# Performance work log

Measured on AMD Instinct MI355X. Metric: run time of the kernel, lower is better.

Reference implementation:

```python
import math
import jax
import jax.numpy as jnp
import numpy as np

B, N, NPOINT, K = 8, 2048, 512, 16
CIN = 64
MLP = [64, 128, 256]
M_W = 8    # PAConv weight-bank size
HID = 16   # scorenet hidden width
GEOM = 10  # 3 rel-xyz + 1 dist + 3 norm + 3 angles


def setup_inputs():
    key = jax.random.key(0)
    ks = jax.random.split(key, 40)
    inp = {}
    inp['xyz'] = jax.random.normal(ks[0], (B, 3, N), jnp.float32)
    inp['norm'] = jax.random.normal(ks[1], (B, 3, N), jnp.float32)
    inp['X_axis'] = jax.random.normal(ks[2], (B, 3, N), jnp.float32)
    inp['Y_axis'] = jax.random.normal(ks[3], (B, 3, N), jnp.float32)
    inp['points'] = jax.random.normal(ks[4], (B, CIN, N), jnp.float32) * 0.5
    cin = CIN
    ki = 5
    for l, cout in enumerate(MLP):
        inp['w1_%d' % l] = jax.random.normal(ks[ki], (HID, GEOM), jnp.float32) / np.sqrt(GEOM); ki += 1
        inp['b1_%d' % l] = jnp.zeros((HID,), jnp.float32)
        inp['w2_%d' % l] = jax.random.normal(ks[ki], (M_W, HID), jnp.float32) / np.sqrt(HID); ki += 1
        inp['b2_%d' % l] = jnp.zeros((M_W,), jnp.float32)
        inp['bank_%d' % l] = jax.random.normal(ks[ki], (M_W, cin, cout), jnp.float32) / np.sqrt(cin); ki += 1
        if l < len(MLP) - 1:
            inp['gamma_%d' % l] = jnp.ones((cout,), jnp.float32)
            inp['beta_%d' % l] = jnp.zeros((cout,), jnp.float32)
        cin = cout
    return inp


def _group(t, idx):
    # t: (B, C, N), idx: (B, ...) int -> (B, C, ...)
    return jax.vmap(lambda p, i: p[:, i])(t, idx)


def _fps(xyz_t, npoint):
    # xyz_t: (B, N, 3) -> (B, npoint) int32; standard iterative FPS starting at index 0
    b, n, _ = xyz_t.shape
    def body(i, c):
        idxs, dists, far = c
        idxs = idxs.at[:, i].set(far)
        centroid = jnp.take_along_axis(xyz_t, far[:, None, None], axis=1)  # (B,1,3)
        d = jnp.sum((xyz_t - centroid) ** 2, axis=-1)
        dists = jnp.minimum(dists, d)
        return idxs, dists, jnp.argmax(dists, axis=-1).astype(jnp.int32)
    idxs = jnp.zeros((b, npoint), jnp.int32)
    dists = jnp.full((b, n), 1e10, xyz_t.dtype)
    far = jnp.zeros((b,), jnp.int32)
    idxs, _, _ = jax.lax.fori_loop(0, npoint, body, (idxs, dists, far))
    return idxs


def _sqdist(a, b):
    # a: (B, P, 3), b: (B, N, 3) -> (B, P, N)
    return (jnp.sum(a ** 2, -1)[:, :, None] + jnp.sum(b ** 2, -1)[:, None, :]
            - 2.0 * jnp.einsum('bpc,bnc->bpn', a, b))


def _angles(gxyz, gn, gX, gY):
    # all (B, 3, P, K) -> (B, 3, P, K); normalized angles to z(norm)/x/y frame axes
    nn = jnp.linalg.norm(gxyz, axis=1)
    def ang(v):
        c = jnp.sum(gxyz * v, axis=1) / (nn * jnp.linalg.norm(v, axis=1) + 1e-8)
        return jnp.arccos(jnp.clip(c, -1.0, 1.0)) / math.pi
    return jnp.stack([ang(gn), ang(gX), ang(gY)], axis=1)


def _paconv(geom, feats, w1, b1, w2, b2, bank, gamma=None, beta=None, act=True):
    # ScoreNet over geometric channels -> softmax scores over M weight matrices
    h = jax.nn.relu(jnp.einsum('hg,bgpk->bhpk', w1, geom) + b1[None, :, None, None])
    s = jax.nn.softmax(jnp.einsum('mh,bhpk->bmpk', w2, h) + b2[None, :, None, None], axis=1)
    out = jnp.einsum('bcpk,mco,bmpk->bopk', feats, bank, s)
    if gamma is not None:
        mu = out.mean(axis=(0, 2, 3), keepdims=True)
        var = out.var(axis=(0, 2, 3), keepdims=True)
        out = (out - mu) / jnp.sqrt(var + 1e-5) * gamma[None, :, None, None] + beta[None, :, None, None]
    return jax.nn.relu(out) if act else out


def reference(xyz, norm, X_axis, Y_axis, points,
              w1_0, b1_0, w2_0, b2_0, bank_0, gamma_0, beta_0,
              w1_1, b1_1, w2_1, b2_1, bank_1, gamma_1, beta_1,
              w1_2, b1_2, w2_2, b2_2, bank_2):
    xyz_t = jnp.transpose(xyz, (0, 2, 1))           # (B,N,3)
    fidx = _fps(xyz_t, NPOINT)                      # (B,NPOINT)
    new_xyz = _group(xyz, fidx)                     # (B,3,NPOINT)
    sq = _sqdist(jnp.transpose(new_xyz, (0, 2, 1)), xyz_t)  # (B,NPOINT,N)
    idx = jax.lax.top_k(-sq, K)[1]                  # (B,NPOINT,K) ascending distance
    grouped_xyz = _group(xyz, idx) - new_xyz[:, :, :, None]  # (B,3,NPOINT,K)
    dist = jnp.sqrt(jnp.sum(grouped_xyz ** 2, axis=1) + 1e-10)  # (B,NPOINT,K)
    dmin = dist.min(axis=2, keepdims=True)
    dist = (dist - dmin) / (dist.max(axis=2, keepdims=True) - dmin + 1e-10)
    new_points = _group(points, idx)                # (B,CIN,NPOINT,K)
    grouped_norm = _group(norm, idx)
    grouped_X = _group(X_axis, idx)
    grouped_Y = _group(Y_axis, idx)
    grouped_angles = _angles(grouped_xyz, grouped_norm, grouped_X, grouped_Y)
    new_norm = grouped_norm[:, :, :, 0]
    new_X = grouped_X[:, :, :, 0]
    new_Y = grouped_Y[:, :, :, 0]
    geom = jnp.concatenate([grouped_xyz, dist[:, None], grouped_norm, grouped_angles], axis=1)  # (B,10,NPOINT,K)
    new_points = _paconv(geom, new_points, w1_0, b1_0, w2_0, b2_0, bank_0, gamma_0, beta_0, act=True)
    new_points = _paconv(geom, new_points, w1_1, b1_1, w2_1, b2_1, bank_1, gamma_1, beta_1, act=True)
    new_points = _paconv(geom, new_points, w1_2, b1_2, w2_2, b2_2, bank_2, None, None, act=False)
    new_points = jnp.max(new_points, axis=3)        # (B,MLP[-1],NPOINT)
    return (new_xyz, new_norm, new_X, new_Y, new_points)
```

## Files before the change

### kernel.cpp

```cpp
#include <hip/hip_runtime.h>
#include <math.h>

#define NBATCH 8
#define NPTS   2048
#define NPOINT 512
#define KNB    16
#define NROWS  (NBATCH*NPOINT*KNB)

typedef unsigned short ushort_t;
typedef unsigned int   uint_t;
typedef unsigned long long ull_t;
typedef __attribute__((ext_vector_type(8))) short  short8;
typedef __attribute__((ext_vector_type(4))) float  f32x4;
typedef __attribute__((ext_vector_type(2))) float  f32x2;

#define B0_OFF 0
#define B1_OFF 32768
#define B2_OFF 98304
#define BT_TOT 360448

#define LDS_BARRIER() asm volatile("s_waitcnt lgkmcnt(0)\n\ts_barrier" ::: "memory")

__device__ __align__(16) int      g_fidx[NBATCH * NPOINT];
__device__ __align__(16) int      g_knn [NROWS];
__device__ __align__(16) float    g_sums[1024];
__device__ __align__(16) float    g_pT  [NBATCH * NPTS * 64];
__device__ __align__(16) float    g_S   [(size_t)3 * NROWS * 8];
__device__ __align__(16) float    g_act1[(size_t)NROWS * 64];
__device__ __align__(16) float    g_act2[(size_t)NROWS * 128];
__device__ __align__(16) ushort_t g_bankF[BT_TOT];

__device__ __forceinline__ ushort_t f2bf(float f) {
    uint_t u = __float_as_uint(f);
    return (ushort_t)((u + 0x7FFFu + ((u >> 16) & 1u)) >> 16);
}

template<int CTRL>
__device__ __forceinline__ ull_t dpp_u64(ull_t k) {
    int lo = (int)(uint_t)k;
    int hi = (int)(uint_t)(k >> 32);
    int slo = __builtin_amdgcn_update_dpp(0, lo, CTRL, 0xF, 0xF, true);
    int shi = __builtin_amdgcn_update_dpp(0, hi, CTRL, 0xF, 0xF, true);
    return ((ull_t)(uint_t)shi << 32) | (uint_t)slo;
}

__device__ __forceinline__ ull_t dpp_max_u64(ull_t key) {
    { ull_t s = dpp_u64<0x111>(key); if (s > key) key = s; }
    { ull_t s = dpp_u64<0x112>(key); if (s > key) key = s; }
    { ull_t s = dpp_u64<0x114>(key); if (s > key) key = s; }
    { ull_t s = dpp_u64<0x118>(key); if (s > key) key = s; }
    { ull_t s = dpp_u64<0x142>(key); if (s > key) key = s; }
    { ull_t s = dpp_u64<0x143>(key); if (s > key) key = s; }
    return key;
}

template<int CTRL>
__device__ __forceinline__ uint_t dpp_u32(uint_t v) {
    return (uint_t)__builtin_amdgcn_update_dpp(0, (int)v, CTRL, 0xF, 0xF, true);
}

__device__ __forceinline__ uint_t dpp_max_u32(uint_t v) {
    { uint_t s = dpp_u32<0x111>(v); if (s > v) v = s; }
    { uint_t s = dpp_u32<0x112>(v); if (s > v) v = s; }
    { uint_t s = dpp_u32<0x114>(v); if (s > v) v = s; }
    { uint_t s = dpp_u32<0x118>(v); if (s > v) v = s; }
    { uint_t s = dpp_u32<0x142>(v); if (s > v) v = s; }
    { uint_t s = dpp_u32<0x143>(v); if (s > v) v = s; }
    return v;
}

template<int COUT>
__device__ __forceinline__ void bank_frag(const float* __restrict__ bank,
                                          ushort_t* __restrict__ dst, int e) {
    const int j = e & 7;
    const int lane = (e >> 3) & 63;
    const int rem = e >> 9;
    constexpr int NTL = COUT / 16;
    const int nt = rem % NTL;
    const int kc = rem / NTL;
    const int q = lane >> 4, nlo = lane & 15;
    const int k = kc * 32 + q * 8 + j;
    const int n = nt * 16 + nlo;
    dst[e] = f2bf(bank[(size_t)k * COUT + n]);
}

__global__ __launch_bounds__(256) void front_kernel(const float* __restrict__ xyz,
                                                    const float* __restrict__ points,
                                                    const float* __restrict__ bank0,
                                                    const float* __restrict__ bank1,
                                                    const float* __restrict__ bank2) {
    __shared__ float smem[4 * NPTS];
    __shared__ ull_t s_key[2][4];
    const int bid = blockIdx.x;
    const int t = threadIdx.x;

    if (bid >= NBATCH) {
        if (bid < NBATCH + 256) {
            float (*tile)[65] = reinterpret_cast<float(*)[65]>(smem);
            const int blk = bid - NBATCH;
            const int b = blk >> 5;
            const int n0 = (blk & 31) * 64;
            const int lane = t & 63, q = t >> 6;
            #pragma unroll
            for (int i = 0; i < 16; ++i) {
                int c = q * 16 + i;
                tile[c][lane] = points[(b * 64 + c) * NPTS + n0 + lane];
            }
            __syncthreads();
            #pragma unroll
            for (int i = 0; i < 16; ++i) {
                int n = q * 16 + i;
                g_pT[(size_t)(b * NPTS + n0 + n) * 64 + lane] = tile[lane][n];
            }
        } else if (bid == NBATCH + 256) {
            g_sums[t] = 0.0f;
            g_sums[256 + t] = 0.0f;
            g_sums[512 + t] = 0.0f;
            g_sums[768 + t] = 0.0f;
        } else {
            const int e = (bid - (NBATCH + 257)) * 256 + t;
            if (e < 32768) {
                bank_frag<64>(bank0, g_bankF + B0_OFF, e);
            } else if (e < 98304) {
                bank_frag<128>(bank1, g_bankF + B1_OFF, e - 32768);
            } else {
                bank_frag<256>(bank2, g_bankF + B2_OFF, e - 98304);
            }
        }
        return;
    }

    {
        #pragma clang fp contract(off)
        const int b = bid;
        const int lane = t & 63, w = t >> 6;
        const float* xb = xyz + b * 3 * NPTS;
        float4* s_pt = reinterpret_cast<float4*>(smem);
        f32x2 xp[4], yp[4], zp[4];
        float d[8];
        {
            const float4* xq = reinterpret_cast<const float4*>(xb + t * 8);
            const float4* yq = reinterpret_cast<const float4*>(xb + NPTS + t * 8);
            const float4* zq = reinterpret_cast<const float4*>(xb + 2 * NPTS + t * 8);
            float4 a0 = xq[0], a1 = xq[1];
            float4 b0 = yq[0], b1 = yq[1];
            float4 c0 = zq[0], c1 = zq[1];
            xp[0] = (f32x2){a0.x, a0.y}; xp[1] = (f32x2){a0.z, a0.w};
            xp[2] = (f32x2){a1.x, a1.y}; xp[3] = (f32x2){a1.z, a1.w};
            yp[0] = (f32x2){b0.x, b0.y}; yp[1] = (f32x2){b0.z, b0.w};
            yp[2] = (f32x2){b1.x, b1.y}; yp[3] = (f32x2){b1.z, b1.w};
            zp[0] = (f32x2){c0.x, c0.y}; zp[1] = (f32x2){c0.z, c0.w};
            zp[2] = (f32x2){c1.x, c1.y}; zp[3] = (f32x2){c1.z, c1.w};
            float4 p0; float4 p1; float4 p2; float4 p3;
            float4 p4; float4 p5; float4 p6; float4 p7;
            p0.x = a0.x; p0.y = b0.x; p0.z = c0.x; p0.w = 0.f;
            p1.x = a0.y; p1.y = b0.y; p1.z = c0.y; p1.w = 0.f;
            p2.x = a0.z; p2.y = b0.z; p2.z = c0.z; p2.w = 0.f;
            p3.x = a0.w; p3.y = b0.w; p3.z = c0.w; p3.w = 0.f;
            p4.x = a1.x; p4.y = b1.x; p4.z = c1.x; p4.w = 0.f;
            p5.x = a1.y; p5.y = b1.y; p5.z = c1.y; p5.w = 0.f;
            p6.x = a1.z; p6.y = b1.z; p6.z = c1.z; p6.w = 0.f;
            p7.x = a1.w; p7.y = b1.w; p7.z = c1.w; p7.w = 0.f;
            s_pt[t * 8 + 0] = p0; s_pt[t * 8 + 1] = p1;
            s_pt[t * 8 + 2] = p2; s_pt[t * 8 + 3] = p3;
            s_pt[t * 8 + 4] = p4; s_pt[t * 8 + 5] = p5;
            s_pt[t * 8 + 6] = p6; s_pt[t * 8 + 7] = p7;
            #pragma unroll
            for (int j = 0; j < 8; ++j) d[j] = 1e10f;
        }
        __syncthreads();
        int far = 0;
        for (int i = 0; i < NPOINT; ++i) {
            if (t == 0) g_fidx[b * NPOINT + i] = far;
            const float4 c4 = s_pt[far];
            const f32x2 cxp = (f32x2){c4.x, c4.x};
            const f32x2 cyp = (f32x2){c4.y, c4.y};
            const f32x2 czp = (f32x2){c4.z, c4.z};
            uint_t bb = 0u;
            #pragma unroll
            for (int a = 0; a < 4; ++a) {
                f32x2 dx = xp[a] - cxp;
                f32x2 dy = yp[a] - cyp;
                f32x2 dz = zp[a] - czp;
                f32x2 s2 = dx*dx + dy*dy;
                s2 = s2 + dz*dz;
                float dn0 = fminf(d[2*a],   s2[0]);
                float dn1 = fminf(d[2*a+1], s2[1]);
                d[2*a] = dn0; d[2*a+1] = dn1;
                uint_t u0 = __float_as_uint(dn0);
                uint_t u1 = __float_as_uint(dn1);
                bb = (u0 > bb) ? u0 : bb;
                bb = (u1 > bb) ? u1 : bb;
            }
            uint_t wm = dpp_max_u32(bb);
            const uint_t wbits = (uint_t)__builtin_amdgcn_readlane((int)wm, 63);
            int li = 8;
            #pragma unroll
            for (int j = 7; j >= 0; --j)
                li = (__float_as_uint(d[j]) == wbits) ? j : li;
            ull_t mk = __ballot(li < 8);
            const int fl = __ffsll((unsigned long long)mk) - 1;
            const int wj = __builtin_amdgcn_readlane(li, fl);
            const int wp = (((w << 6) + fl) << 3) + wj;
            if (lane == 0) s_key[i & 1][w] = ((ull_t)wbits << 32) | (uint_t)(~wp);
            LDS_BARRIER();
            const ull_t* kb = s_key[i & 1];
            ull_t k0 = kb[0], k1 = kb[1], k2 = kb[2], k3 = kb[3];
            if (k1 > k0) k0 = k1;
            if (k3 > k2) k2 = k3;
            if (k2 > k0) k0 = k2;
            far = (int)(~(uint_t)k0) & (NPTS - 1);
        }
    }
}

__global__ __launch_bounds__(256) void knn_score_kernel(
    const float* __restrict__ xyz, const float* __restrict__ nrm,
    const float* __restrict__ Xa, const float* __restrict__ Ya,
    const float* __restrict__ w1_0, const float* __restrict__ b1_0,
    const float* __restrict__ w2_0, const float* __restrict__ b2_0,
    const float* __restrict__ w1_1, const float* __restrict__ b1_1,
    const float* __restrict__ w2_1, const float* __restrict__ b2_1,
    const float* __restrict__ w1_2, const float* __restrict__ b1_2,
    const float* __restrict__ w2_2, const float* __restrict__ b2_2) {
    __shared__ float w1s[3][16][10];
    __shared__ float b1s[3][16];
    __shared__ float w2s[3][8][16];
    __shared__ float b2s[3][8];
    const int t = threadIdx.x;
    {
        const float* w1p[3] = {w1_0, w1_1, w1_2};
        const float* b1p[3] = {b1_0, b1_1, b1_2};
        const float* w2p[3] = {w2_0, w2_1, w2_2};
        const float* b2p[3] = {b2_0, b2_1, b2_2};
        #pragma unroll
        for (int l = 0; l < 3; ++l) {
            if (t < 160) w1s[l][t / 10][t % 10] = w1p[l][t];
            if (t < 16)  b1s[l][t] = b1p[l][t];
            if (t < 128) w2s[l][t / 16][t % 16] = w2p[l][t];
            if (t < 8)   b2s[l][t] = b2p[l][t];
        }
    }
    __syncthreads();

    const int wave = blockIdx.x * 4 + (t >> 6);
    const int lane = t & 63;
    const int b = wave >> 9;
    const float* xb = xyz + b * 3 * NPTS;
    const int fi = g_fidx[wave] & (NPTS - 1);
    int nmine = 0;

    {
        #pragma clang fp contract(off)
        float ax = xb[fi];
        float ay = xb[NPTS + fi];
        float az = xb[2*NPTS + fi];
        float sa = ax*ax + ay*ay; sa = sa + az*az;
        float d[32];
        #pragma unroll
        for (int j = 0; j < 32; ++j) {
            int pp = j * 64 + lane;
            float bx = xb[pp];
            float by = xb[NPTS + pp];
            float bz = xb[2*NPTS + pp];
            float sb = bx*bx + by*by; sb = sb + bz*bz;
            float dot = ax*bx + ay*by; dot = dot + az*bz;
            float t1 = sa + sb;
            float t2 = 2.0f * dot;
            d[j] = t1 - t2;
        }
        for (int r = 0; r < KNB; ++r) {
            float best = 1e30f; int bi = 0x7fffffff;
            #pragma unroll
            for (int j = 0; j < 32; ++j) {
                if (d[j] < best) { best = d[j]; bi = j * 64 + lane; }
            }
            uint_t ub = __float_as_uint(best);
            ub = (ub & 0x80000000u) ? ~ub : (ub | 0x80000000u);
            ull_t key = ((ull_t)(~ub) << 32) | (uint_t)(~bi);
            key = dpp_max_u64(key);
            uint_t wlo = (uint_t)__builtin_amdgcn_readlane((int)(uint_t)key, 63);
            bi = (int)(~wlo) & (NPTS - 1);
            if (lane == 0) g_knn[wave * KNB + r] = bi;
            if (lane == r) nmine = bi;
            int rl = bi & 63, rs = bi >> 6;
            if (lane == rl) {
                #pragma unroll
                for (int j = 0; j < 32; ++j) if (j == rs) d[j] = 1e30f;
            }
        }
    }

    if (lane < 16) {
        const int row = wave * KNB + lane;
        const int n = nmine & (NPTS - 1);
        const float* nb = nrm + b * 3 * NPTS;
        const float* Xb = Xa  + b * 3 * NPTS;
        const float* Yb = Ya  + b * 3 * NPTS;
        float gx, gy, gz, sq, draw, nnv;
        {
            #pragma clang fp contract(off)
            gx = xb[n]        - xb[fi];
            gy = xb[NPTS + n] - xb[NPTS + fi];
            gz = xb[2*NPTS+n] - xb[2*NPTS+fi];
            sq = gx*gx + gy*gy;
            sq = sq + gz*gz;
            draw = sqrtf(sq + 1e-10f);
            nnv = sqrtf(sq);
        }
        float dmin = draw, dmax = draw;
        #pragma unroll
        for (int m = 1; m < 16; m <<= 1) {
            dmin = fminf(dmin, __shfl_xor(dmin, m, 16));
            dmax = fmaxf(dmax, __shfl_xor(dmax, m, 16));
        }
        float dist;
        {
            #pragma clang fp contract(off)
            dist = (draw - dmin) / ((dmax - dmin) + 1e-10f);
        }
        float nx = nb[n], ny = nb[NPTS+n], nz = nb[2*NPTS+n];
        float Xx = Xb[n], Xy = Xb[NPTS+n], Xz = Xb[2*NPTS+n];
        float Yx = Yb[n], Yy = Yb[NPTS+n], Yz = Yb[2*NPTS+n];
        float g[10];
        g[0]=gx; g[1]=gy; g[2]=gz; g[3]=dist; g[4]=nx; g[5]=ny; g[6]=nz;
        {
            float vs[3][3] = {{nx,ny,nz},{Xx,Xy,Xz},{Yx,Yy,Yz}};
            #pragma unroll
            for (int a = 0; a < 3; ++a) {
                float vx=vs[a][0], vy=vs[a][1], vz=vs[a][2];
                float dot, nv;
                {
                    #pragma clang fp contract(off)
                    dot = gx*vx + gy*vy; dot = dot + gz*vz;
                    float s2 = vx*vx + vy*vy; s2 = s2 + vz*vz;
                    nv = sqrtf(s2);
                }
                float cc = dot / (nnv * nv + 1e-8f);
                cc = fminf(1.0f, fmaxf(-1.0f, cc));
                g[7+a] = acosf(cc) / 3.14159274101257324f;
            }
        }
        #pragma unroll
        for (int l = 0; l < 3; ++l) {
            float h[16];
            #pragma unroll
            for (int i = 0; i < 16; ++i) {
                float a = b1s[l][i];
                #pragma unroll
                for (int j = 0; j < 10; ++j) a += w1s[l][i][j] * g[j];
                h[i] = fmaxf(a, 0.0f);
            }
            float e[8]; float mx = -1e30f;
            #pragma unroll
            for (int m = 0; m < 8; ++m) {
                float a = b2s[l][m];
                #pragma unroll
                for (int j = 0; j < 16; ++j) a += w2s[l][m][j] * h[j];
                e[m] = a; mx = fmaxf(mx, a);
            }
            float sum = 0.0f;
            #pragma unroll
            for (int m = 0; m < 8; ++m) { e[m] = expf(e[m] - mx); sum += e[m]; }
            #pragma unroll
            for (int m = 0; m < 8; ++m)
                g_S[(size_t)l * NROWS * 8 + (size_t)row * 8 + m] = e[m] / sum;
        }
    }
}

template<int LAYER, int CIN, int COUT>
__global__ __launch_bounds__(256) void gemm_kernel(const float* __restrict__ gamma,
                                                   const float* __restrict__ beta,
                                                   float* __restrict__ dout,
                                                   const float* __restrict__ xyz,
                                                   const float* __restrict__ nrm,
                                                   const float* __restrict__ Xa,
                                                   const float* __restrict__ Ya) {
    if constexpr (LAYER == 0) {
        if (blockIdx.x >= 1024) {
            const int g = (blockIdx.x - 1024) * 256 + threadIdx.x;
            const int b = g / NPOINT, p = g % NPOINT;
            const int fi = g_fidx[g] & (NPTS - 1);
            const int n0 = g_knn[g * KNB] & (NPTS - 1);
            #pragma unroll
            for (int a = 0; a < 3; ++a) {
                dout[            (b*3 + a) * NPOINT + p] = xyz[(b*3 + a) * NPTS + fi];
                dout[12288 +     (b*3 + a) * NPOINT + p] = nrm[(b*3 + a) * NPTS + n0];
                dout[24576 +     (b*3 + a) * NPOINT + p] = Xa [(b*3 + a) * NPTS + n0];
                dout[36864 +     (b*3 + a) * NPOINT + p] = Ya [(b*3 + a) * NPTS + n0];
            }
            return;
        }
    }

    const float* __restrict__ A = (LAYER == 0) ? g_pT : (LAYER == 1) ? g_act1 : g_act2;
    float* __restrict__ O = (LAYER == 0) ? g_act1 : (LAYER == 1) ? g_act2 : dout;
    constexpr int NTT = COUT / 16;
    constexpr int NTW = NTT / 4;
    constexpr int CCM = CIN / 32;
    constexpr int BOFF = (LAYER == 0) ? B0_OFF : (LAYER == 1) ? B1_OFF : B2_OFF;
    __shared__ ushort_t As[2][64][36];
    __shared__ float s_scale[(LAYER >= 1) ? CIN : 1];
    __shared__ float s_shift[(LAYER >= 1) ? CIN : 1];
    __shared__ float s_rs[(LAYER < 2) ? COUT : 1];
    __shared__ float s_rss[(LAYER < 2) ? COUT : 1];

    const int t = threadIdx.x;
    const int lane = t & 63, w = t >> 6;
    const int q = lane >> 4, nlo = lane & 15;
    const int row0 = blockIdx.x * 64;
    const int arow_i = t >> 2, acg = t & 3;

    if constexpr (LAYER >= 1) {
        const float* sb = (LAYER == 1) ? g_sums : (g_sums + 256);
        if (t < CIN) {
            float mu  = sb[t] * (1.0f / 65536.0f);
            float var = sb[CIN + t] * (1.0f / 65536.0f) - mu * mu;
            var = fmaxf(var, 0.0f);
            float sc = gamma[t] / sqrtf(var + 1e-5f);
            s_scale[t] = sc;
            s_shift[t] = beta[t] - mu * sc;
        }
        __syncthreads();
    }

    size_t arow;
    if (LAYER == 0) {
        const int row = row0 + arow_i;
        const int b = row >> 13;
        const int n = g_knn[row] & (NPTS - 1);
        arow = (size_t)(b * NPTS + n) * 64;
    } else {
        arow = (size_t)(row0 + arow_i) * CIN;
    }
    const float* Sbase = g_S + (size_t)LAYER * NROWS * 8 + (size_t)(row0 + arow_i) * 8;

    float svv[8];
    #pragma unroll
    for (int m = 0; m < 8; ++m) svv[m] = Sbase[m];

    f32x4 acc[4][NTW];
    #pragma unroll
    for (int mi = 0; mi < 4; ++mi)
        #pragma unroll
        for (int ni = 0; ni < NTW; ++ni) acc[mi][ni] = (f32x4){0.f, 0.f, 0.f, 0.f};

    const ushort_t* fbase = g_bankF + BOFF + lane * 8;

    union FragU { uint4 u4; uint2 u2[2]; short8 s; };
    FragU B[2][NTW];
    #pragma unroll
    for (int ni = 0; ni < NTW; ++ni)
        B[0][ni].u4 = *reinterpret_cast<const uint4*>(fbase + (size_t)(w * NTW + ni) * 512);

    float vraw[8], vnext[8];
    {
        const float* ap = A + arow + acg * 8;
        float4 fa = *reinterpret_cast<const float4*>(ap);
        float4 fb = *reinterpret_cast<const float4*>(ap + 4);
        vraw[0]=fa.x; vraw[1]=fa.y; vraw[2]=fa.z; vraw[3]=fa.w;
        vraw[4]=fb.x; vraw[5]=fb.y; vraw[6]=fb.z; vraw[7]=fb.w;
    }

    int par = 0;
    for (int cc = 0; cc < CCM; ++cc) {
        float v[8];
        #pragma unroll
        for (int j = 0; j < 8; ++j) {
            if constexpr (LAYER >= 1) {
                const int c = cc * 32 + acg * 8 + j;
                v[j] = fmaxf(vraw[j] * s_scale[c] + s_shift[c], 0.f);
            } else {
                v[j] = vraw[j];
            }
        }
        #pragma unroll
        for (int m = 0; m < 8; ++m) {
            {
                const float sv = svv[m];
                uint_t* dst = reinterpret_cast<uint_t*>(&As[par][arow_i][acg * 8]);
                #pragma unroll
                for (int j = 0; j < 8; j += 2)
                    dst[j >> 1] = (uint_t)f2bf(sv * v[j]) | ((uint_t)f2bf(sv * v[j+1]) << 16);
            }
            if (m == 0) {
                const int ccn = (cc + 1 < CCM) ? cc + 1 : cc;
                const float* ap = A + arow + ccn * 32 + acg * 8;
                float4 fa = *reinterpret_cast<const float4*>(ap);
                float4 fb = *reinterpret_cast<const float4*>(ap + 4);
                vnext[0]=fa.x; vnext[1]=fa.y; vnext[2]=fa.z; vnext[3]=fa.w;
                vnext[4]=fb.x; vnext[5]=fb.y; vnext[6]=fb.z; vnext[7]=fb.w;
            }
            {
                const int kcn = (m < 7) ? ((m + 1) * CCM + cc)
                                        : ((cc + 1 < CCM) ? (cc + 1) : 0);
                #pragma unroll
                for (int ni = 0; ni < NTW; ++ni)
                    B[(m + 1) & 1][ni].u4 = *reinterpret_cast<const uint4*>(
                        fbase + (size_t)(kcn * NTT + w * NTW + ni) * 512);
            }
            LDS_BARRIER();
            FragU af[4];
            #pragma unroll
            for (int mi = 0; mi < 4; ++mi) {
                af[mi].u2[0] = *reinterpret_cast<const uint2*>(&As[par][mi*16 + nlo][q*8]);
                af[mi].u2[1] = *reinterpret_cast<const uint2*>(&As[par][mi*16 + nlo][q*8 + 4]);
            }
            #pragma unroll
            for (int ni = 0; ni < NTW; ++ni)
                #pragma unroll
                for (int mi = 0; mi < 4; ++mi)
                    acc[mi][ni] = __builtin_amdgcn_mfma_f32_16x16x32_bf16(
                        af[mi].s, B[m & 1][ni].s, acc[mi][ni], 0, 0, 0);
            par ^= 1;
        }
        #pragma unroll
        for (int j = 0; j < 8; ++j) vraw[j] = vnext[j];
    }

    if constexpr (LAYER == 2) {
        const int bp0 = row0 >> 4;
        #pragma unroll
        for (int mi = 0; mi < 4; ++mi) {
            const int bp = bp0 + mi;
            const int b = bp >> 9, p = bp & 511;
            #pragma unroll
            for (int ni = 0; ni < NTW; ++ni) {
                float mv = fmaxf(fmaxf(acc[mi][ni][0], acc[mi][ni][1]),
                                 fmaxf(acc[mi][ni][2], acc[mi][ni][3]));
                mv = fmaxf(mv, __shfl_xor(mv, 16));
                mv = fmaxf(mv, __shfl_xor(mv, 32));
                if (lane < 16) {
                    const int col = w * 64 + ni * 16 + nlo;
                    O[(size_t)(b * 256 + col) * NPOINT + p] = mv;
                }
            }
        }
    } else {
        #pragma unroll
        for (int mi = 0; mi < 4; ++mi)
            #pragma unroll
            for (int ni = 0; ni < NTW; ++ni)
                #pragma unroll
                for (int r2 = 0; r2 < 4; ++r2)
                    O[(size_t)(row0 + mi*16 + q*4 + r2) * COUT + w*NTW*16 + ni*16 + nlo] = acc[mi][ni][r2];
        #pragma unroll
        for (int ni = 0; ni < NTW; ++ni) {
            float s = 0.f, ss = 0.f;
            #pragma unroll
            for (int mi = 0; mi < 4; ++mi) {
                #pragma unroll
                for (int r2 = 0; r2 < 4; ++r2) {
                    float x = acc[mi][ni][r2];
                    s += x; ss += x * x;
                }
            }
            s  += __shfl_xor(s, 16);  s  += __shfl_xor(s, 32);
            ss += __shfl_xor(ss, 16); ss += __shfl_xor(ss, 32);
            if (q == 0) {
                const int c = w * NTW * 16 + ni * 16 + nlo;
                s_rs[c] = s;
                s_rss[c] = ss;
            }
        }
        __syncthreads();
        if (t < COUT) {
            float* sb = (LAYER == 0) ? g_sums : (g_sums + 256);
            atomicAdd(&sb[t], s_rs[t]);
            atomicAdd(&sb[COUT + t], s_rss[t]);
        }
    }
}

extern "C" void kernel_launch(void* const* d_in, const int* in_sizes, int n_in,
                              void* d_out, int out_size, void* d_ws, size_t ws_size,
                              hipStream_t stream) {
    const float* xyz    = (const float*)d_in[0];
    const float* nrm    = (const float*)d_in[1];
    const float* Xa     = (const float*)d_in[2];
    const float* Ya     = (const float*)d_in[3];
    const float* points = (const float*)d_in[4];
    const float* w1_0 = (const float*)d_in[5];  const float* b1_0 = (const float*)d_in[6];
    const float* w2_0 = (const float*)d_in[7];  const float* b2_0 = (const float*)d_in[8];
    const float* bank0 = (const float*)d_in[9];
    const float* g0 = (const float*)d_in[10];   const float* be0 = (const float*)d_in[11];
    const float* w1_1 = (const float*)d_in[12]; const float* b1_1 = (const float*)d_in[13];
    const float* w2_1 = (const float*)d_in[14]; const float* b2_1 = (const float*)d_in[15];
    const float* bank1 = (const float*)d_in[16];
    const float* g1 = (const float*)d_in[17];   const float* be1 = (const float*)d_in[18];
    const float* w1_2 = (const float*)d_in[19]; const float* b1_2 = (const float*)d_in[20];
    const float* w2_2 = (const float*)d_in[21]; const float* b2_2 = (const float*)d_in[22];
    const float* bank2 = (const float*)d_in[23];
    float* out = (float*)d_out;
    (void)d_ws; (void)ws_size; (void)in_sizes; (void)n_in; (void)out_size;

    front_kernel<<<1673, 256, 0, stream>>>(xyz, points, bank0, bank1, bank2);
    knn_score_kernel<<<1024, 256, 0, stream>>>(xyz, nrm, Xa, Ya,
                                               w1_0, b1_0, w2_0, b2_0,
                                               w1_1, b1_1, w2_1, b2_1,
                                               w1_2, b1_2, w2_2, b2_2);
    gemm_kernel<0, 64, 64><<<1040, 256, 0, stream>>>(nullptr, nullptr, out, xyz, nrm, Xa, Ya);
    gemm_kernel<1, 64, 128><<<1024, 256, 0, stream>>>(g0, be0, nullptr, nullptr, nullptr, nullptr, nullptr);
    gemm_kernel<2, 128, 256><<<1024, 256, 0, stream>>>(g1, be1, out + 49152, nullptr, nullptr, nullptr, nullptr);
}
```

Baseline: 461.6 us.

## Fuse FPS and KNN/scorenet into one kernel with per-centroid ready flags

Merges the front kernel (FPS, transpose, bank conversion) and the KNN/scorenet kernel into one launch. KNN waves spin on per-centroid ready flags that the FPS blocks publish each iteration, so neighbour search and scoring overlap the serial FPS loop instead of waiting for it to finish. The FPS shared-memory layout also changes from padded float4 to SoA. The risks are deadlock if KNN blocks occupy every slot before the FPS blocks are scheduled, the cost of spin-polling, and the relaxed atomics giving no ordering guarantee on g_fidx.

```diff
diff --git a/kernel.cpp b/kernel.cpp
--- a/kernel.cpp
+++ b/kernel.cpp
@@ -6,6 +6,12 @@
 #define NPOINT 512
 #define KNB    16
 #define NROWS  (NBATCH*NPOINT*KNB)
+
+#define TRANS_BASE  NBATCH
+#define ZERO_BID    (NBATCH + 256)
+#define CONV_BASE   (NBATCH + 257)
+#define KNN_BASE    (NBATCH + 257 + 1408)
+#define MEGA_GRID   (KNN_BASE + 1024)
 
 typedef unsigned short ushort_t;
 typedef unsigned int   uint_t;
@@ -21,7 +27,8 @@
 
 #define LDS_BARRIER() asm volatile("s_waitcnt lgkmcnt(0)\n\ts_barrier" ::: "memory")
 
-__device__ __align__(16) int      g_fidx[NBATCH * NPOINT];
+__device__ __align__(16) int      g_fidx [NBATCH * NPOINT];
+__device__ __align__(16) int      g_fready[NBATCH * NPOINT];
 __device__ __align__(16) int      g_knn [NROWS];
 __device__ __align__(16) float    g_sums[1024];
 __device__ __align__(16) float    g_pT  [NBATCH * NPTS * 64];
@@ -84,20 +91,27 @@
     dst[e] = f2bf(bank[(size_t)k * COUT + n]);
 }
 
-__global__ __launch_bounds__(256) void front_kernel(const float* __restrict__ xyz,
-                                                    const float* __restrict__ points,
-                                                    const float* __restrict__ bank0,
-                                                    const float* __restrict__ bank1,
-                                                    const float* __restrict__ bank2) {
-    __shared__ float smem[4 * NPTS];
+__global__ __launch_bounds__(256, 5) void mega_kernel(
+    const float* __restrict__ xyz, const float* __restrict__ points,
+    const float* __restrict__ bank0, const float* __restrict__ bank1,
+    const float* __restrict__ bank2,
+    const float* __restrict__ nrm, const float* __restrict__ Xa,
+    const float* __restrict__ Ya,
+    const float* __restrict__ w1_0, const float* __restrict__ b1_0,
+    const float* __restrict__ w2_0, const float* __restrict__ b2_0,
+    const float* __restrict__ w1_1, const float* __restrict__ b1_1,
+    const float* __restrict__ w2_1, const float* __restrict__ b2_1,
+    const float* __restrict__ w1_2, const float* __restrict__ b1_2,
+    const float* __restrict__ w2_2, const float* __restrict__ b2_2) {
+    __shared__ float smem[3 * NPTS];
     __shared__ ull_t s_key[2][4];
     const int bid = blockIdx.x;
     const int t = threadIdx.x;
 
     if (bid >= NBATCH) {
-        if (bid < NBATCH + 256) {
+        if (bid < ZERO_BID) {
             float (*tile)[65] = reinterpret_cast<float(*)[65]>(smem);
-            const int blk = bid - NBATCH;
+            const int blk = bid - TRANS_BASE;
             const int b = blk >> 5;
             const int n0 = (blk & 31) * 64;
             const int lane = t & 63, q = t >> 6;
@@ -112,13 +126,15 @@
                 int n = q * 16 + i;
                 g_pT[(size_t)(b * NPTS + n0 + n) * 64 + lane] = tile[lane][n];
             }
-        } else if (bid == NBATCH + 256) {
+            return;
+        } else if (bid == ZERO_BID) {
             g_sums[t] = 0.0f;
             g_sums[256 + t] = 0.0f;
             g_sums[512 + t] = 0.0f;
             g_sums[768 + t] = 0.0f;
-        } else {
-            const int e = (bid - (NBATCH + 257)) * 256 + t;
+            return;
+        } else if (bid < KNN_BASE) {
+            const int e = (bid - CONV_BASE) * 256 + t;
             if (e < 32768) {
                 bank_frag<64>(bank0, g_bankF + B0_OFF, e);
             } else if (e < 98304) {
@@ -126,6 +142,158 @@
             } else {
                 bank_frag<256>(bank2, g_bankF + B2_OFF, e - 98304);
             }
+            return;
+        }
+
+        {
+            const float* w1p[3] = {w1_0, w1_1, w1_2};
+            const float* b1p[3] = {b1_0, b1_1, b1_2};
+            const float* w2p[3] = {w2_0, w2_1, w2_2};
+            const float* b2p[3] = {b2_0, b2_1, b2_2};
+            #pragma unroll
+            for (int l = 0; l < 3; ++l) {
+                if (t < 160) smem[l * 160 + t] = w1p[l][t];
+                if (t < 16)  smem[480 + l * 16 + t] = b1p[l][t];
+                if (t < 128) smem[528 + l * 128 + t] = w2p[l][t];
+                if (t < 8)   smem[912 + l * 8 + t] = b2p[l][t];
+            }
+        }
+        __syncthreads();
+
+        const int wave = (bid - KNN_BASE) * 4 + (t >> 6);
+        const int lane = t & 63;
+        const int b = wave >> 9;
+        const float* xb = xyz + b * 3 * NPTS;
+
+        int fv = __hip_atomic_load(&g_fready[wave], __ATOMIC_RELAXED,
+                                   __HIP_MEMORY_SCOPE_AGENT);
+        while (fv == 0) {
+            __builtin_amdgcn_s_sleep(8);
+            fv = __hip_atomic_load(&g_fready[wave], __ATOMIC_RELAXED,
+                                   __HIP_MEMORY_SCOPE_AGENT);
+        }
+        if (lane == 0)
+            __hip_atomic_store(&g_fready[wave], 0, __ATOMIC_RELAXED,
+                               __HIP_MEMORY_SCOPE_AGENT);
+        const int fi = (fv - 1) & (NPTS - 1);
+        int nmine = 0;
+
+        {
+            #pragma clang fp contract(off)
+            float ax = xb[fi];
+            float ay = xb[NPTS + fi];
+            float az = xb[2*NPTS + fi];
+            float sa = ax*ax + ay*ay; sa = sa + az*az;
+            float d[32];
+            #pragma unroll
+            for (int j = 0; j < 32; ++j) {
+                int pp = j * 64 + lane;
+                float bx = xb[pp];
+                float by = xb[NPTS + pp];
+                float bz = xb[2*NPTS + pp];
+                float sb = bx*bx + by*by; sb = sb + bz*bz;
+                float dot = ax*bx + ay*by; dot = dot + az*bz;
+                float t1 = sa + sb;
+                float t2 = 2.0f * dot;
+                d[j] = t1 - t2;
+            }
+            for (int r = 0; r < KNB; ++r) {
+                float best = 1e30f; int bi = 0x7fffffff;
+                #pragma unroll
+                for (int j = 0; j < 32; ++j) {
+                    if (d[j] < best) { best = d[j]; bi = j * 64 + lane; }
+                }
+                uint_t ub = __float_as_uint(best);
+                ub = (ub & 0x80000000u) ? ~ub : (ub | 0x80000000u);
+                ull_t key = ((ull_t)(~ub) << 32) | (uint_t)(~bi);
+                key = dpp_max_u64(key);
+                uint_t wlo = (uint_t)__builtin_amdgcn_readlane((int)(uint_t)key, 63);
+                bi = (int)(~wlo) & (NPTS - 1);
+                if (lane == 0) g_knn[wave * KNB + r] = bi;
+                if (lane == r) nmine = bi;
+                int rl = bi & 63, rs = bi >> 6;
+                if (lane == rl) {
+                    #pragma unroll
+                    for (int j = 0; j < 32; ++j) if (j == rs) d[j] = 1e30f;
+                }
+            }
+        }
+
+        if (lane < 16) {
+            const int row = wave * KNB + lane;
+            const int n = nmine & (NPTS - 1);
+            const float* nb = nrm + b * 3 * NPTS;
+            const float* Xb = Xa  + b * 3 * NPTS;
+            const float* Yb = Ya  + b * 3 * NPTS;
+            float gx, gy, gz, sq, draw, nnv;
+            {
+                #pragma clang fp contract(off)
+                gx = xb[n]        - xb[fi];
+                gy = xb[NPTS + n] - xb[NPTS + fi];
+                gz = xb[2*NPTS+n] - xb[2*NPTS+fi];
+                sq = gx*gx + gy*gy;
+                sq = sq + gz*gz;
+                draw = sqrtf(sq + 1e-10f);
+                nnv = sqrtf(sq);
+            }
+            float dmin = draw, dmax = draw;
+            #pragma unroll
+            for (int m = 1; m < 16; m <<= 1) {
+                dmin = fminf(dmin, __shfl_xor(dmin, m, 16));
+                dmax = fmaxf(dmax, __shfl_xor(dmax, m, 16));
+            }
+            float dist;
+            {
+                #pragma clang fp contract(off)
+                dist = (draw - dmin) / ((dmax - dmin) + 1e-10f);
+            }
+            float nx = nb[n], ny = nb[NPTS+n], nz = nb[2*NPTS+n];
+            float Xx = Xb[n], Xy = Xb[NPTS+n], Xz = Xb[2*NPTS+n];
+            float Yx = Yb[n], Yy = Yb[NPTS+n], Yz = Yb[2*NPTS+n];
+            float g[10];
+            g[0]=gx; g[1]=gy; g[2]=gz; g[3]=dist; g[4]=nx; g[5]=ny; g[6]=nz;
+            {
+                float vs[3][3] = {{nx,ny,nz},{Xx,Xy,Xz},{Yx,Yy,Yz}};
+                #pragma unroll
+                for (int a = 0; a < 3; ++a) {
+                    float vx=vs[a][0], vy=vs[a][1], vz=vs[a][2];
+                    float dot, nv;
+                    {
+                        #pragma clang fp contract(off)
+                        dot = gx*vx + gy*vy; dot = dot + gz*vz;
+                        float s2 = vx*vx + vy*vy; s2 = s2 + vz*vz;
+                        nv = sqrtf(s2);
+                    }
+                    float cc = dot / (nnv * nv + 1e-8f);
+                    cc = fminf(1.0f, fmaxf(-1.0f, cc));
+                    g[7+a] = acosf(cc) / 3.14159274101257324f;
+                }
+            }
+            #pragma unroll
+            for (int l = 0; l < 3; ++l) {
+                float h[16];
+                #pragma unroll
+                for (int i = 0; i < 16; ++i) {
+                    float a = smem[480 + l * 16 + i];
+                    #pragma unroll
+                    for (int j = 0; j < 10; ++j) a += smem[l * 160 + i * 10 + j] * g[j];
+                    h[i] = fmaxf(a, 0.0f);
+                }
+                float e[8]; float mx = -1e30f;
+                #pragma unroll
+                for (int m = 0; m < 8; ++m) {
+                    float a = smem[912 + l * 8 + m];
+                    #pragma unroll
+                    for (int j = 0; j < 16; ++j) a += smem[528 + l * 128 + m * 16 + j] * h[j];
+                    e[m] = a; mx = fmaxf(mx, a);
+                }
+                float sum = 0.0f;
+                #pragma unroll
+                for (int m = 0; m < 8; ++m) { e[m] = expf(e[m] - mx); sum += e[m]; }
+                #pragma unroll
+                for (int m = 0; m < 8; ++m)
+                    g_S[(size_t)l * NROWS * 8 + (size_t)row * 8 + m] = e[m] / sum;
+            }
         }
         return;
     }
@@ -135,7 +303,9 @@
         const int b = bid;
         const int lane = t & 63, w = t >> 6;
         const float* xb = xyz + b * 3 * NPTS;
-        float4* s_pt = reinterpret_cast<float4*>(smem);
+        float* s_x = smem;
+        float* s_y = smem + NPTS;
+        float* s_z = smem + 2 * NPTS;
         f32x2 xp[4], yp[4], zp[4];
         float d[8];
         {
@@ -151,31 +321,27 @@
             yp[2] = (f32x2){b1.x, b1.y}; yp[3] = (f32x2){b1.z, b1.w};
             zp[0] = (f32x2){c0.x, c0.y}; zp[1] = (f32x2){c0.z, c0.w};
             zp[2] = (f32x2){c1.x, c1.y}; zp[3] = (f32x2){c1.z, c1.w};
-            float4 p0; float4 p1; float4 p2; float4 p3;
-            float4 p4; float4 p5; float4 p6; float4 p7;
-            p0.x = a0.x; p0.y = b0.x; p0.z = c0.x; p0.w = 0.f;
-            p1.x = a0.y; p1.y = b0.y; p1.z = c0.y; p1.w = 0.f;
-            p2.x = a0.z; p2.y = b0.z; p2.z = c0.z; p2.w = 0.f;
-            p3.x = a0.w; p3.y = b0.w; p3.z = c0.w; p3.w = 0.f;
-            p4.x = a1.x; p4.y = b1.x; p4.z = c1.x; p4.w = 0.f;
-            p5.x = a1.y; p5.y = b1.y; p5.z = c1.y; p5.w = 0.f;
-            p6.x = a1.z; p6.y = b1.z; p6.z = c1.z; p6.w = 0.f;
-            p7.x = a1.w; p7.y = b1.w; p7.z = c1.w; p7.w = 0.f;
-            s_pt[t * 8 + 0] = p0; s_pt[t * 8 + 1] = p1;
-            s_pt[t * 8 + 2] = p2; s_pt[t * 8 + 3] = p3;
-            s_pt[t * 8 + 4] = p4; s_pt[t * 8 + 5] = p5;
-            s_pt[t * 8 + 6] = p6; s_pt[t * 8 + 7] = p7;
+            *reinterpret_cast<float4*>(s_x + t * 8)     = a0;
+            *reinterpret_cast<float4*>(s_x + t * 8 + 4) = a1;
+            *reinterpret_cast<float4*>(s_y + t * 8)     = b0;
+            *reinterpret_cast<float4*>(s_y + t * 8 + 4) = b1;
+            *reinterpret_cast<float4*>(s_z + t * 8)     = c0;
+            *reinterpret_cast<float4*>(s_z + t * 8 + 4) = c1;
             #pragma unroll
             for (int j = 0; j < 8; ++j) d[j] = 1e10f;
         }
         __syncthreads();
         int far = 0;
         for (int i = 0; i < NPOINT; ++i) {
-            if (t == 0) g_fidx[b * NPOINT + i] = far;
-            const float4 c4 = s_pt[far];
-            const f32x2 cxp = (f32x2){c4.x, c4.x};
-            const f32x2 cyp = (f32x2){c4.y, c4.y};
-            const f32x2 czp = (f32x2){c4.z, c4.z};
+            if (t == 0) {
+                g_fidx[b * NPOINT + i] = far;
+                __hip_atomic_store(&g_fready[b * NPOINT + i], far + 1,
+                                   __ATOMIC_RELAXED, __HIP_MEMORY_SCOPE_AGENT);
+            }
+            const float cx = s_x[far], cy = s_y[far], cz = s_z[far];
+            const f32x2 cxp = (f32x2){cx, cx};
+            const f32x2 cyp = (f32x2){cy, cy};
+            const f32x2 czp = (f32x2){cz, cz};
             uint_t bb = 0u;
             #pragma unroll
             for (int a = 0; a < 4; ++a) {
@@ -210,161 +376,6 @@
             if (k3 > k2) k2 = k3;
             if (k2 > k0) k0 = k2;
             far = (int)(~(uint_t)k0) & (NPTS - 1);
-        }
-    }
-}
-
-__global__ __launch_bounds__(256) void knn_score_kernel(
-    const float* __restrict__ xyz, const float* __restrict__ nrm,
-    const float* __restrict__ Xa, const float* __restrict__ Ya,
-    const float* __restrict__ w1_0, const float* __restrict__ b1_0,
-    const float* __restrict__ w2_0, const float* __restrict__ b2_0,
-    const float* __restrict__ w1_1, const float* __restrict__ b1_1,
-    const float* __restrict__ w2_1, const float* __restrict__ b2_1,
-    const float* __restrict__ w1_2, const float* __restrict__ b1_2,
-    const float* __restrict__ w2_2, const float* __restrict__ b2_2) {
-    __shared__ float w1s[3][16][10];
-    __shared__ float b1s[3][16];
-    __shared__ float w2s[3][8][16];
-    __shared__ float b2s[3][8];
-    const int t = threadIdx.x;
-    {
-        const float* w1p[3] = {w1_0, w1_1, w1_2};
-        const float* b1p[3] = {b1_0, b1_1, b1_2};
-        const float* w2p[3] = {w2_0, w2_1, w2_2};
-        const float* b2p[3] = {b2_0, b2_1, b2_2};
-        #pragma unroll
-        for (int l = 0; l < 3; ++l) {
-            if (t < 160) w1s[l][t / 10][t % 10] = w1p[l][t];
-            if (t < 16)  b1s[l][t] = b1p[l][t];
-            if (t < 128) w2s[l][t / 16][t % 16] = w2p[l][t];
-            if (t < 8)   b2s[l][t] = b2p[l][t];
-        }
-    }
-    __syncthreads();
-
-    const int wave = blockIdx.x * 4 + (t >> 6);
-    const int lane = t & 63;
-    const int b = wave >> 9;
-    const float* xb = xyz + b * 3 * NPTS;
-    const int fi = g_fidx[wave] & (NPTS - 1);
-    int nmine = 0;
-
-    {
-        #pragma clang fp contract(off)
-        float ax = xb[fi];
-        float ay = xb[NPTS + fi];
-        float az = xb[2*NPTS + fi];
-        float sa = ax*ax + ay*ay; sa = sa + az*az;
-        float d[32];
-        #pragma unroll
-        for (int j = 0; j < 32; ++j) {
-            int pp = j * 64 + lane;
-            float bx = xb[pp];
-            float by = xb[NPTS + pp];
-            float bz = xb[2*NPTS + pp];
-            float sb = bx*bx + by*by; sb = sb + bz*bz;
-            float dot = ax*bx + ay*by; dot = dot + az*bz;
-            float t1 = sa + sb;
-            float t2 = 2.0f * dot;
-            d[j] = t1 - t2;
-        }
-        for (int r = 0; r < KNB; ++r) {
-            float best = 1e30f; int bi = 0x7fffffff;
-            #pragma unroll
-            for (int j = 0; j < 32; ++j) {
-                if (d[j] < best) { best = d[j]; bi = j * 64 + lane; }
-            }
-            uint_t ub = __float_as_uint(best);
-            ub = (ub & 0x80000000u) ? ~ub : (ub | 0x80000000u);
-            ull_t key = ((ull_t)(~ub) << 32) | (uint_t)(~bi);
-            key = dpp_max_u64(key);
-            uint_t wlo = (uint_t)__builtin_amdgcn_readlane((int)(uint_t)key, 63);
-            bi = (int)(~wlo) & (NPTS - 1);
-            if (lane == 0) g_knn[wave * KNB + r] = bi;
-            if (lane == r) nmine = bi;
-            int rl = bi & 63, rs = bi >> 6;
-            if (lane == rl) {
-                #pragma unroll
-                for (int j = 0; j < 32; ++j) if (j == rs) d[j] = 1e30f;
-            }
-        }
-    }
-
-    if (lane < 16) {
-        const int row = wave * KNB + lane;
-        const int n = nmine & (NPTS - 1);
-        const float* nb = nrm + b * 3 * NPTS;
-        const float* Xb = Xa  + b * 3 * NPTS;
-        const float* Yb = Ya  + b * 3 * NPTS;
-        float gx, gy, gz, sq, draw, nnv;
-        {
-            #pragma clang fp contract(off)
-            gx = xb[n]        - xb[fi];
-            gy = xb[NPTS + n] - xb[NPTS + fi];
-            gz = xb[2*NPTS+n] - xb[2*NPTS+fi];
-            sq = gx*gx + gy*gy;
-            sq = sq + gz*gz;
-            draw = sqrtf(sq + 1e-10f);
-            nnv = sqrtf(sq);
-        }
-        float dmin = draw, dmax = draw;
-        #pragma unroll
-        for (int m = 1; m < 16; m <<= 1) {
-            dmin = fminf(dmin, __shfl_xor(dmin, m, 16));
-            dmax = fmaxf(dmax, __shfl_xor(dmax, m, 16));
-        }
-        float dist;
-        {
-            #pragma clang fp contract(off)
-            dist = (draw - dmin) / ((dmax - dmin) + 1e-10f);
-        }
-        float nx = nb[n], ny = nb[NPTS+n], nz = nb[2*NPTS+n];
-        float Xx = Xb[n], Xy = Xb[NPTS+n], Xz = Xb[2*NPTS+n];
-        float Yx = Yb[n], Yy = Yb[NPTS+n], Yz = Yb[2*NPTS+n];
-        float g[10];
-        g[0]=gx; g[1]=gy; g[2]=gz; g[3]=dist; g[4]=nx; g[5]=ny; g[6]=nz;
-        {
-            float vs[3][3] = {{nx,ny,nz},{Xx,Xy,Xz},{Yx,Yy,Yz}};
-            #pragma unroll
-            for (int a = 0; a < 3; ++a) {
-                float vx=vs[a][0], vy=vs[a][1], vz=vs[a][2];
-                float dot, nv;
-                {
-                    #pragma clang fp contract(off)
-                    dot = gx*vx + gy*vy; dot = dot + gz*vz;
-                    float s2 = vx*vx + vy*vy; s2 = s2 + vz*vz;
-                    nv = sqrtf(s2);
-                }
-                float cc = dot / (nnv * nv + 1e-8f);
-                cc = fminf(1.0f, fmaxf(-1.0f, cc));
-                g[7+a] = acosf(cc) / 3.14159274101257324f;
-            }
-        }
-        #pragma unroll
-        for (int l = 0; l < 3; ++l) {
-            float h[16];
-            #pragma unroll
-            for (int i = 0; i < 16; ++i) {
-                float a = b1s[l][i];
-                #pragma unroll
-                for (int j = 0; j < 10; ++j) a += w1s[l][i][j] * g[j];
-                h[i] = fmaxf(a, 0.0f);
-            }
-            float e[8]; float mx = -1e30f;
-            #pragma unroll
-            for (int m = 0; m < 8; ++m) {
-                float a = b2s[l][m];
-                #pragma unroll
-                for (int j = 0; j < 16; ++j) a += w2s[l][m][j] * h[j];
-                e[m] = a; mx = fmaxf(mx, a);
-            }
-            float sum = 0.0f;
-            #pragma unroll
-            for (int m = 0; m < 8; ++m) { e[m] = expf(e[m] - mx); sum += e[m]; }
-            #pragma unroll
-            for (int m = 0; m < 8; ++m)
-                g_S[(size_t)l * NROWS * 8 + (size_t)row * 8 + m] = e[m] / sum;
         }
     }
 }
@@ -595,8 +606,8 @@
     float* out = (float*)d_out;
     (void)d_ws; (void)ws_size; (void)in_sizes; (void)n_in; (void)out_size;
 
-    front_kernel<<<1673, 256, 0, stream>>>(xyz, points, bank0, bank1, bank2);
-    knn_score_kernel<<<1024, 256, 0, stream>>>(xyz, nrm, Xa, Ya,
+    mega_kernel<<<MEGA_GRID, 256, 0, stream>>>(xyz, points, bank0, bank1, bank2,
+                                               nrm, Xa, Ya,
                                                w1_0, b1_0, w2_0, b2_0,
                                                w1_1, b1_1, w2_1, b2_1,
                                                w1_2, b1_2, w2_2, b2_2);
```

Result: faster. 443.7 us (-3.9%).
